# Performance work log

Hardware: AMD Instinct MI355X
Metric: run time of the kernel (lower is better)

## Reference

```python
import jax, jax.numpy as jnp
import numpy as np


def setup_inputs() -> dict:
    key = jax.random.key(0)
    k1, k2 = jax.random.split(key)
    B, C, H, L = 4, 1, 1024, 4096
    x = jax.random.normal(k1, (B, H, L), dtype=jnp.float32)
    k = jax.random.normal(k2, (C, H, L), dtype=jnp.float32)
    return {"x": x, "k": k}


def reference(x, k):
    # x: (B, H, L) input; k: (C, H, l_kernel) SSM convolution kernel.
    # FFT convolution with zero-padding to n = l_kernel + L (linear conv),
    # then truncate to the first L outputs (causal conv output).
    L = x.shape[-1]
    l_kernel = k.shape[-1]
    n = l_kernel + L
    k_f = jnp.fft.rfft(k, n=n)                       # (C, H, n//2+1) complex
    x_f = jnp.fft.rfft(x, n=n)                       # (B, H, n//2+1) complex
    y_f = jnp.einsum('bhl,chl->bchl', x_f, k_f)      # broadcast complex multiply
    y = jnp.fft.irfft(y_f, n=n)[..., :L]             # (B, C, H, L)
    return y
```

## Files before the change

### kernel.cpp

```cpp
#include <hip/hip_runtime.h>

#define THREADS 256
#define B_DIM   4
#define H_DIM   1024
#define L_DIM   4096
#define NFFT    4096
#define PI_F     3.14159265358979323846f
#define TWO_PI_F 6.28318530717958647692f

__device__ __forceinline__ float2 cmulf(float2 a, float2 b) {
    return make_float2(a.x*b.x - a.y*b.y, a.x*b.y + a.y*b.x);
}
__device__ __forceinline__ float2 caddf(float2 a, float2 b){ return make_float2(a.x+b.x, a.y+b.y); }
__device__ __forceinline__ float2 csubf(float2 a, float2 b){ return make_float2(a.x-b.x, a.y-b.y); }

__device__ __forceinline__ int swz(int i) { return i ^ ((i>>4)&15) ^ ((i>>8)&15); }

__device__ __forceinline__ void make_tw(float base, float2 w[16]) {
    float sn, cs; __sincosf(base, &sn, &cs);
    w[1]  = make_float2(cs, sn);
    w[2]  = cmulf(w[1], w[1]);
    w[3]  = cmulf(w[2], w[1]);
    w[4]  = cmulf(w[2], w[2]);
    w[5]  = cmulf(w[4], w[1]);
    w[6]  = cmulf(w[4], w[2]);
    w[7]  = cmulf(w[4], w[3]);
    w[8]  = cmulf(w[4], w[4]);
    w[9]  = cmulf(w[8], w[1]);
    w[10] = cmulf(w[8], w[2]);
    w[11] = cmulf(w[8], w[3]);
    w[12] = cmulf(w[8], w[4]);
    w[13] = cmulf(w[8], w[5]);
    w[14] = cmulf(w[8], w[6]);
    w[15] = cmulf(w[8], w[7]);
}

__device__ __forceinline__ float2 w16c(int q, float s) {
    constexpr float C[8] = {1.f, 0.9238795325f, 0.7071067812f, 0.3826834324f,
                            0.f, -0.3826834324f, -0.7071067812f, -0.9238795325f};
    constexpr float S[8] = {0.f, 0.3826834324f, 0.7071067812f, 0.9238795325f,
                            1.f, 0.9238795325f, 0.7071067812f, 0.3826834324f};
    return make_float2(C[q], s*S[q]);
}

template<int SGN>
__device__ __forceinline__ float2 twq(float2 d, int q) {
    if (q == 0) return d;
    if (q == 4) return make_float2((float)(-SGN)*d.y, (float)SGN*d.x);
    return cmulf(d, w16c(q, (float)SGN));
}

template<int SGN, bool HZ>
__device__ __forceinline__ void dif16(float2 v[16]) {
    if (HZ) {
        #pragma unroll
        for (int i = 0; i < 8; ++i) {
            float2 a = v[i];
            v[i+8] = twq<SGN>(a, i);
        }
    } else {
        #pragma unroll
        for (int i = 0; i < 8; ++i) {
            float2 a = v[i], b = v[i+8];
            v[i]   = caddf(a,b);
            v[i+8] = twq<SGN>(csubf(a,b), i);
        }
    }
    #pragma unroll
    for (int h = 4; h >= 1; h >>= 1) {
        const int step = 8 / h;
        #pragma unroll
        for (int g = 0; g < 16; g += 2*h) {
            #pragma unroll
            for (int i = 0; i < h; ++i) {
                float2 a = v[g+i], b = v[g+i+h];
                v[g+i]   = caddf(a,b);
                v[g+i+h] = twq<SGN>(csubf(a,b), i*step);
            }
        }
    }
}

template<int SGN>
__device__ __forceinline__ void dit16(float2 v[16]) {
    #pragma unroll
    for (int h = 1; h <= 8; h <<= 1) {
        const int step = 8 / h;
        #pragma unroll
        for (int g = 0; g < 16; g += 2*h) {
            #pragma unroll
            for (int i = 0; i < h; ++i) {
                float2 a = v[g+i];
                float2 b = twq<SGN>(v[g+i+h], i*step);
                v[g+i]   = caddf(a,b);
                v[g+i+h] = csubf(a,b);
            }
        }
    }
}

__device__ __constant__ int REV4_C[16] = {0,8,4,12,2,10,6,14,1,9,5,13,3,11,7,15};

__device__ __forceinline__ void fwd_fft_row(const float2* __restrict__ src, float2* Z, int t) {
    constexpr int REV4[16] = {0,8,4,12,2,10,6,14,1,9,5,13,3,11,7,15};
    float2 v[16], w[16];
    #pragma unroll
    for (int r = 0; r < 8; ++r) v[r] = src[256*r + t];
    dif16<-1, true>(v);
    make_tw(-TWO_PI_F * (float)t / (float)NFFT, w);
    #pragma unroll
    for (int kk = 1; kk < 16; ++kk) v[REV4[kk]] = cmulf(v[REV4[kk]], w[kk]);
    #pragma unroll
    for (int kk = 0; kk < 16; ++kk) Z[swz(256*kk + t)] = v[REV4[kk]];
    __syncthreads();

    const int k1 = t >> 4, m = t & 15;
    const int rb = 256*k1 + m;
    #pragma unroll
    for (int r = 0; r < 16; ++r) v[r] = Z[swz(rb + 16*r)];
    dif16<-1,false>(v);
    make_tw(-TWO_PI_F * (float)m / 256.f, w);
    #pragma unroll
    for (int kk = 1; kk < 16; ++kk) v[REV4[kk]] = cmulf(v[REV4[kk]], w[kk]);
    #pragma unroll
    for (int kk = 0; kk < 16; ++kk) Z[swz(rb + 16*kk)] = v[REV4[kk]];
    __syncthreads();

    const int b3 = t << 4;
    #pragma unroll
    for (int r = 0; r < 16; ++r) v[r] = Z[swz(b3 + r)];
    dif16<-1,false>(v);
    #pragma unroll
    for (int kk = 0; kk < 16; ++kk) Z[swz(b3 + kk)] = v[REV4[kk]];
}

__device__ __forceinline__ int binpos(int j) {
    return swz( ((j&15)<<8) | (((j>>4)&15)<<4) | (j>>8) );
}

__global__ __launch_bounds__(THREADS, 4)
void kfft_kernel(const float* __restrict__ k, float2* __restrict__ Kf_all) {
    __shared__ float2 Zk[NFFT];
    const int t  = threadIdx.x;
    const int hh = blockIdx.x;
    const float2* kp = (const float2*)(k + (size_t)hh * L_DIM);

    fwd_fft_row(kp, Zk, t);
    __syncthreads();

    float2* Kf = Kf_all + (size_t)hh * NFFT;
    #pragma unroll
    for (int s = 0; s < 8; ++s) {
        int j = t + 256*s;
        if (j == 0) {
            float2 zk = Zk[0];
            Kf[0] = make_float2(zk.x + zk.y, zk.x - zk.y);
            float2 zk2 = Zk[swz(8)];
            Kf[2048] = make_float2(zk2.x, -zk2.y);
        } else {
            int jm = NFFT - j;
            float2 zkj = Zk[binpos(j)], zkm = Zk[binpos(jm)];
            float sn, cs; __sincosf(-PI_F * (float)j / (float)NFFT, &sn, &cs);
            float2 w = make_float2(cs, sn);
            float2 Ke = make_float2(0.5f*(zkj.x + zkm.x), 0.5f*(zkj.y - zkm.y));
            float2 dk = make_float2(zkj.x - zkm.x, zkj.y + zkm.y);
            float2 Ko = make_float2(0.5f*dk.y, -0.5f*dk.x);
            float2 tk = cmulf(w, Ko);
            Kf[j]  = caddf(Ke, tk);
            Kf[jm] = make_float2(Ke.x - tk.x, -(Ke.y - tk.y));
        }
    }
}

__global__ __launch_bounds__(THREADS, 4)
void conv_main_kernel(const float* __restrict__ x, const float2* __restrict__ Kf_all,
                      float* __restrict__ out) {
    __shared__ float2 Zx[NFFT];
    constexpr int REV4[16] = {0,8,4,12,2,10,6,14,1,9,5,13,3,11,7,15};

    const int t  = threadIdx.x;
    const int wg = blockIdx.x;
    const int hh = wg & (H_DIM - 1);
    const int b  = wg >> 10;

    const float2* xp = (const float2*)(x + ((size_t)(b*H_DIM + hh)) * L_DIM);
    const float2* Kf = Kf_all + (size_t)hh * NFFT;

    fwd_fft_row(xp, Zx, t);

    float2 kfj[8], kfm[8], kf2;
    #pragma unroll
    for (int s = 0; s < 8; ++s) {
        int j = t + 256*s;
        kfj[s] = Kf[j];
        kfm[s] = Kf[(NFFT - j) & (NFFT - 1)];
    }
    kf2 = Kf[2048];
    __syncthreads();

    #pragma unroll
    for (int s = 0; s < 8; ++s) {
        int j = t + 256*s;
        if (j == 0) {
            float2 zx = Zx[0];
            float ax0 = zx.x + zx.y, axM = zx.x - zx.y;
            float y0 = ax0 * kfj[0].x, yM = axM * kfj[0].y;
            Zx[0] = make_float2(0.5f*(y0 + yM), 0.5f*(y0 - yM));
            int p2 = swz(8);
            float2 zx2 = Zx[p2];
            Zx[p2] = cmulf(zx2, make_float2(kf2.x, -kf2.y));
        } else {
            int jm = NFFT - j;
            int pj = binpos(j), pm = binpos(jm);
            float2 zxj = Zx[pj], zxm = Zx[pm];

            float sn, cs; __sincosf(-PI_F * (float)j / (float)NFFT, &sn, &cs);
            float2 w = make_float2(cs, sn);

            float2 Xe = make_float2(0.5f*(zxj.x + zxm.x), 0.5f*(zxj.y - zxm.y));
            float2 dx = make_float2(zxj.x - zxm.x, zxj.y + zxm.y);
            float2 Xo = make_float2(0.5f*dx.y, -0.5f*dx.x);
            float2 tx = cmulf(w, Xo);
            float2 Axj = caddf(Xe, tx);
            float2 Axm = make_float2(Xe.x - tx.x, -(Xe.y - tx.y));

            float2 Yj = cmulf(Axj, kfj[s]);
            float2 Ym = cmulf(Axm, kfm[s]);

            float2 u  = make_float2(0.5f*(Yj.x + Ym.x), 0.5f*(Yj.y - Ym.y));
            float2 dd = make_float2(Yj.x - Ym.x, Yj.y + Ym.y);
            float2 wc = make_float2(w.x, -w.y);
            float2 vv = cmulf(wc, dd);
            vv.x *= 0.5f; vv.y *= 0.5f;
            Zx[pj] = make_float2(u.x - vv.y, u.y + vv.x);
            Zx[pm] = make_float2(u.x + vv.y, -(u.y - vv.x));
        }
    }
    __syncthreads();

    float2 vx[16], w[16];
    const int k1 = t >> 4, m = t & 15;
    const int rb = 256*k1 + m;
    const int b3 = t << 4;

    #pragma unroll
    for (int r = 0; r < 16; ++r) vx[REV4[r]] = Zx[swz(b3 + r)];
    dit16<1>(vx);
    #pragma unroll
    for (int mm = 0; mm < 16; ++mm) Zx[swz(b3 + mm)] = vx[mm];
    __syncthreads();

    make_tw(TWO_PI_F * (float)m / 256.f, w);
    #pragma unroll
    for (int kk = 0; kk < 16; ++kk) {
        float2 val = Zx[swz(rb + 16*kk)];
        if (kk > 0) val = cmulf(val, w[kk]);
        vx[REV4[kk]] = val;
    }
    dit16<1>(vx);
    #pragma unroll
    for (int r = 0; r < 16; ++r) Zx[swz(rb + 16*r)] = vx[r];
    __syncthreads();

    make_tw(TWO_PI_F * (float)t / (float)NFFT, w);
    #pragma unroll
    for (int kk = 0; kk < 16; ++kk) {
        float2 val = Zx[swz(256*kk + t)];
        if (kk > 0) val = cmulf(val, w[kk]);
        vx[REV4[kk]] = val;
    }
    dit16<1>(vx);
    float2* op = (float2*)(out + ((size_t)(b*H_DIM + hh)) * L_DIM);
    const float sc = 1.f / (float)NFFT;
    #pragma unroll
    for (int n1 = 0; n1 < 8; ++n1) {
        float2 z = vx[n1];
        op[256*n1 + t] = make_float2(z.x*sc, z.y*sc);
    }
}

__global__ __launch_bounds__(THREADS, 2)
void fftconv_fallback(const float* __restrict__ x, const float* __restrict__ k,
                      float* __restrict__ out) {
    __shared__ float2 Zx[NFFT];
    __shared__ float2 Zk[NFFT];
    constexpr int REV4[16] = {0,8,4,12,2,10,6,14,1,9,5,13,3,11,7,15};

    const int t  = threadIdx.x;
    const int wg = blockIdx.x;
    const int hh = wg & (H_DIM - 1);
    const int b  = wg >> 10;

    const float2* xp = (const float2*)(x + ((size_t)(b*H_DIM + hh)) * L_DIM);
    const float2* kp = (const float2*)(k + (size_t)hh * L_DIM);

    fwd_fft_row(xp, Zx, t);
    __syncthreads();
    fwd_fft_row(kp, Zk, t);
    __syncthreads();

    #pragma unroll
    for (int s = 0; s < 8; ++s) {
        int j = t + 256*s;
        if (j == 0) {
            float2 zx = Zx[0], zk = Zk[0];
            float ax0 = zx.x + zx.y, axM = zx.x - zx.y;
            float ak0 = zk.x + zk.y, akM = zk.x - zk.y;
            float y0 = ax0*ak0, yM = axM*akM;
            Zx[0] = make_float2(0.5f*(y0+yM), 0.5f*(y0-yM));
            int p2 = swz(8);
            Zx[p2] = cmulf(Zx[p2], Zk[p2]);
        } else {
            int jm = NFFT - j;
            int pj = binpos(j), pm = binpos(jm);
            float2 zxj = Zx[pj], zxm = Zx[pm];
            float2 zkj = Zk[pj], zkm = Zk[pm];
            float sn, cs; __sincosf(-PI_F * (float)j / (float)NFFT, &sn, &cs);
            float2 w = make_float2(cs, sn);
            float2 Xe = make_float2(0.5f*(zxj.x + zxm.x), 0.5f*(zxj.y - zxm.y));
            float2 dx = make_float2(zxj.x - zxm.x, zxj.y + zxm.y);
            float2 Xo = make_float2(0.5f*dx.y, -0.5f*dx.x);
            float2 tx = cmulf(w, Xo);
            float2 Axj = caddf(Xe, tx);
            float2 Axm = make_float2(Xe.x - tx.x, -(Xe.y - tx.y));
            float2 Ke = make_float2(0.5f*(zkj.x + zkm.x), 0.5f*(zkj.y - zkm.y));
            float2 dk = make_float2(zkj.x - zkm.x, zkj.y + zkm.y);
            float2 Ko = make_float2(0.5f*dk.y, -0.5f*dk.x);
            float2 tk = cmulf(w, Ko);
            float2 Akj = caddf(Ke, tk);
            float2 Akm = make_float2(Ke.x - tk.x, -(Ke.y - tk.y));
            float2 Yj = cmulf(Axj, Akj);
            float2 Ym = cmulf(Axm, Akm);
            float2 u  = make_float2(0.5f*(Yj.x + Ym.x), 0.5f*(Yj.y - Ym.y));
            float2 dd = make_float2(Yj.x - Ym.x, Yj.y + Ym.y);
            float2 wc = make_float2(w.x, -w.y);
            float2 vv = cmulf(wc, dd);
            vv.x *= 0.5f; vv.y *= 0.5f;
            Zx[pj] = make_float2(u.x - vv.y, u.y + vv.x);
            Zx[pm] = make_float2(u.x + vv.y, -(u.y - vv.x));
        }
    }
    __syncthreads();

    float2 vx[16], w[16];
    const int k1 = t >> 4, m = t & 15;
    const int rb = 256*k1 + m;
    const int b3 = t << 4;

    #pragma unroll
    for (int r = 0; r < 16; ++r) vx[REV4[r]] = Zx[swz(b3 + r)];
    dit16<1>(vx);
    #pragma unroll
    for (int mm = 0; mm < 16; ++mm) Zx[swz(b3 + mm)] = vx[mm];
    __syncthreads();

    make_tw(TWO_PI_F * (float)m / 256.f, w);
    #pragma unroll
    for (int kk = 0; kk < 16; ++kk) {
        float2 val = Zx[swz(rb + 16*kk)];
        if (kk > 0) val = cmulf(val, w[kk]);
        vx[REV4[kk]] = val;
    }
    dit16<1>(vx);
    #pragma unroll
    for (int r = 0; r < 16; ++r) Zx[swz(rb + 16*r)] = vx[r];
    __syncthreads();

    make_tw(TWO_PI_F * (float)t / (float)NFFT, w);
    #pragma unroll
    for (int kk = 0; kk < 16; ++kk) {
        float2 val = Zx[swz(256*kk + t)];
        if (kk > 0) val = cmulf(val, w[kk]);
        vx[REV4[kk]] = val;
    }
    dit16<1>(vx);
    float2* op = (float2*)(out + ((size_t)(b*H_DIM + hh)) * L_DIM);
    const float sc = 1.f / (float)NFFT;
    #pragma unroll
    for (int n1 = 0; n1 < 8; ++n1) {
        float2 z = vx[n1];
        op[256*n1 + t] = make_float2(z.x*sc, z.y*sc);
    }
}

extern "C" void kernel_launch(void* const* d_in, const int* in_sizes, int n_in,
                              void* d_out, int out_size, void* d_ws, size_t ws_size,
                              hipStream_t stream) {
    const float* x = (const float*)d_in[0];
    const float* k = (const float*)d_in[1];
    float* out = (float*)d_out;
    const size_t need = (size_t)H_DIM * NFFT * sizeof(float2);
    if (ws_size >= need) {
        float2* Kf = (float2*)d_ws;
        kfft_kernel<<<dim3(H_DIM), dim3(THREADS), 0, stream>>>(k, Kf);
        conv_main_kernel<<<dim3(B_DIM * H_DIM), dim3(THREADS), 0, stream>>>(x, Kf, out);
    } else {
        fftconv_fallback<<<dim3(B_DIM * H_DIM), dim3(THREADS), 0, stream>>>(x, k, out);
    }
}
```

Measured before the change: 176.4 us.

## Fuse kernel FFT into conv kernel, looping over batch per head

Replaces the two-kernel scheme (kernel FFT written to workspace, then per-batch conv) with one kernel per head. Each block computes the k spectrum into registers once and reuses it across all four batch rows, which removes the workspace round trip and the second launch. It also replaces the per-bin sincos with a twiddle recurrence and skips the unused upper half of the final inverse butterfly. The cost is that the grid shrinks from 4096 to 1024 blocks with serial batch work per block, which lowers parallelism, and the recurrence may add rounding drift.

```diff
diff --git a/kernel.cpp b/kernel.cpp
--- a/kernel.cpp
+++ b/kernel.cpp
@@ -81,10 +81,10 @@
     }
 }
 
-template<int SGN>
+template<int SGN, bool HALF>
 __device__ __forceinline__ void dit16(float2 v[16]) {
     #pragma unroll
-    for (int h = 1; h <= 8; h <<= 1) {
+    for (int h = 1; h <= 4; h <<= 1) {
         const int step = 8 / h;
         #pragma unroll
         for (int g = 0; g < 16; g += 2*h) {
@@ -97,9 +97,14 @@
             }
         }
     }
-}
-
-__device__ __constant__ int REV4_C[16] = {0,8,4,12,2,10,6,14,1,9,5,13,3,11,7,15};
+    #pragma unroll
+    for (int i = 0; i < 8; ++i) {
+        float2 a = v[i];
+        float2 b = twq<SGN>(v[i+8], i);
+        v[i] = caddf(a,b);
+        if (!HALF) v[i+8] = csubf(a,b);
+    }
+}
 
 __device__ __forceinline__ void fwd_fft_row(const float2* __restrict__ src, float2* Z, int t) {
     constexpr int REV4[16] = {0,8,4,12,2,10,6,14,1,9,5,13,3,11,7,15};
@@ -138,248 +143,138 @@
     return swz( ((j&15)<<8) | (((j>>4)&15)<<4) | (j>>8) );
 }
 
+#define WSTEP_RE 0.980785280403230449f
+#define WSTEP_IM -0.195090322016128268f
+
 __global__ __launch_bounds__(THREADS, 4)
-void kfft_kernel(const float* __restrict__ k, float2* __restrict__ Kf_all) {
-    __shared__ float2 Zk[NFFT];
+void fftconv_fused(const float* __restrict__ x, const float* __restrict__ k,
+                   float* __restrict__ out) {
+    __shared__ float2 Z[NFFT];
+    constexpr int REV4[16] = {0,8,4,12,2,10,6,14,1,9,5,13,3,11,7,15};
+
     const int t  = threadIdx.x;
     const int hh = blockIdx.x;
+
     const float2* kp = (const float2*)(k + (size_t)hh * L_DIM);
-
-    fwd_fft_row(kp, Zk, t);
-    __syncthreads();
-
-    float2* Kf = Kf_all + (size_t)hh * NFFT;
-    #pragma unroll
-    for (int s = 0; s < 8; ++s) {
-        int j = t + 256*s;
-        if (j == 0) {
-            float2 zk = Zk[0];
-            Kf[0] = make_float2(zk.x + zk.y, zk.x - zk.y);
-            float2 zk2 = Zk[swz(8)];
-            Kf[2048] = make_float2(zk2.x, -zk2.y);
-        } else {
-            int jm = NFFT - j;
-            float2 zkj = Zk[binpos(j)], zkm = Zk[binpos(jm)];
-            float sn, cs; __sincosf(-PI_F * (float)j / (float)NFFT, &sn, &cs);
-            float2 w = make_float2(cs, sn);
-            float2 Ke = make_float2(0.5f*(zkj.x + zkm.x), 0.5f*(zkj.y - zkm.y));
-            float2 dk = make_float2(zkj.x - zkm.x, zkj.y + zkm.y);
-            float2 Ko = make_float2(0.5f*dk.y, -0.5f*dk.x);
-            float2 tk = cmulf(w, Ko);
-            Kf[j]  = caddf(Ke, tk);
-            Kf[jm] = make_float2(Ke.x - tk.x, -(Ke.y - tk.y));
-        }
-    }
-}
-
-__global__ __launch_bounds__(THREADS, 4)
-void conv_main_kernel(const float* __restrict__ x, const float2* __restrict__ Kf_all,
-                      float* __restrict__ out) {
-    __shared__ float2 Zx[NFFT];
-    constexpr int REV4[16] = {0,8,4,12,2,10,6,14,1,9,5,13,3,11,7,15};
-
-    const int t  = threadIdx.x;
-    const int wg = blockIdx.x;
-    const int hh = wg & (H_DIM - 1);
-    const int b  = wg >> 10;
-
-    const float2* xp = (const float2*)(x + ((size_t)(b*H_DIM + hh)) * L_DIM);
-    const float2* Kf = Kf_all + (size_t)hh * NFFT;
-
-    fwd_fft_row(xp, Zx, t);
+    fwd_fft_row(kp, Z, t);
+    __syncthreads();
 
     float2 kfj[8], kfm[8], kf2;
-    #pragma unroll
-    for (int s = 0; s < 8; ++s) {
-        int j = t + 256*s;
-        kfj[s] = Kf[j];
-        kfm[s] = Kf[(NFFT - j) & (NFFT - 1)];
-    }
-    kf2 = Kf[2048];
-    __syncthreads();
-
-    #pragma unroll
-    for (int s = 0; s < 8; ++s) {
-        int j = t + 256*s;
-        if (j == 0) {
-            float2 zx = Zx[0];
-            float ax0 = zx.x + zx.y, axM = zx.x - zx.y;
-            float y0 = ax0 * kfj[0].x, yM = axM * kfj[0].y;
-            Zx[0] = make_float2(0.5f*(y0 + yM), 0.5f*(y0 - yM));
-            int p2 = swz(8);
-            float2 zx2 = Zx[p2];
-            Zx[p2] = cmulf(zx2, make_float2(kf2.x, -kf2.y));
-        } else {
-            int jm = NFFT - j;
-            int pj = binpos(j), pm = binpos(jm);
-            float2 zxj = Zx[pj], zxm = Zx[pm];
-
-            float sn, cs; __sincosf(-PI_F * (float)j / (float)NFFT, &sn, &cs);
-            float2 w = make_float2(cs, sn);
-
-            float2 Xe = make_float2(0.5f*(zxj.x + zxm.x), 0.5f*(zxj.y - zxm.y));
-            float2 dx = make_float2(zxj.x - zxm.x, zxj.y + zxm.y);
-            float2 Xo = make_float2(0.5f*dx.y, -0.5f*dx.x);
-            float2 tx = cmulf(w, Xo);
-            float2 Axj = caddf(Xe, tx);
-            float2 Axm = make_float2(Xe.x - tx.x, -(Xe.y - tx.y));
-
-            float2 Yj = cmulf(Axj, kfj[s]);
-            float2 Ym = cmulf(Axm, kfm[s]);
-
-            float2 u  = make_float2(0.5f*(Yj.x + Ym.x), 0.5f*(Yj.y - Ym.y));
-            float2 dd = make_float2(Yj.x - Ym.x, Yj.y + Ym.y);
-            float2 wc = make_float2(w.x, -w.y);
-            float2 vv = cmulf(wc, dd);
-            vv.x *= 0.5f; vv.y *= 0.5f;
-            Zx[pj] = make_float2(u.x - vv.y, u.y + vv.x);
-            Zx[pm] = make_float2(u.x + vv.y, -(u.y - vv.x));
-        }
-    }
-    __syncthreads();
-
-    float2 vx[16], w[16];
+    {
+        float sn, cs; __sincosf(-PI_F * (float)t / (float)NFFT, &sn, &cs);
+        float2 wj = make_float2(cs, sn);
+        const float2 WS = make_float2(WSTEP_RE, WSTEP_IM);
+        kf2 = Z[swz(8)];
+        #pragma unroll
+        for (int s = 0; s < 8; ++s) {
+            int j = t + 256*s;
+            if (j == 0) {
+                float2 zk = Z[0];
+                kfj[0] = make_float2(zk.x + zk.y, zk.x - zk.y);
+                kfm[0] = make_float2(0.f, 0.f);
+            } else {
+                int jm = NFFT - j;
+                float2 zkj = Z[binpos(j)], zkm = Z[binpos(jm)];
+                float2 Ke = make_float2(0.5f*(zkj.x + zkm.x), 0.5f*(zkj.y - zkm.y));
+                float2 dk = make_float2(zkj.x - zkm.x, zkj.y + zkm.y);
+                float2 Ko = make_float2(0.5f*dk.y, -0.5f*dk.x);
+                float2 tk = cmulf(wj, Ko);
+                kfj[s] = caddf(Ke, tk);
+                kfm[s] = make_float2(Ke.x - tk.x, -(Ke.y - tk.y));
+            }
+            wj = cmulf(wj, WS);
+        }
+    }
+    __syncthreads();
+
     const int k1 = t >> 4, m = t & 15;
     const int rb = 256*k1 + m;
     const int b3 = t << 4;
 
-    #pragma unroll
-    for (int r = 0; r < 16; ++r) vx[REV4[r]] = Zx[swz(b3 + r)];
-    dit16<1>(vx);
-    #pragma unroll
-    for (int mm = 0; mm < 16; ++mm) Zx[swz(b3 + mm)] = vx[mm];
-    __syncthreads();
-
-    make_tw(TWO_PI_F * (float)m / 256.f, w);
-    #pragma unroll
-    for (int kk = 0; kk < 16; ++kk) {
-        float2 val = Zx[swz(rb + 16*kk)];
-        if (kk > 0) val = cmulf(val, w[kk]);
-        vx[REV4[kk]] = val;
-    }
-    dit16<1>(vx);
-    #pragma unroll
-    for (int r = 0; r < 16; ++r) Zx[swz(rb + 16*r)] = vx[r];
-    __syncthreads();
-
-    make_tw(TWO_PI_F * (float)t / (float)NFFT, w);
-    #pragma unroll
-    for (int kk = 0; kk < 16; ++kk) {
-        float2 val = Zx[swz(256*kk + t)];
-        if (kk > 0) val = cmulf(val, w[kk]);
-        vx[REV4[kk]] = val;
-    }
-    dit16<1>(vx);
-    float2* op = (float2*)(out + ((size_t)(b*H_DIM + hh)) * L_DIM);
-    const float sc = 1.f / (float)NFFT;
-    #pragma unroll
-    for (int n1 = 0; n1 < 8; ++n1) {
-        float2 z = vx[n1];
-        op[256*n1 + t] = make_float2(z.x*sc, z.y*sc);
-    }
-}
-
-__global__ __launch_bounds__(THREADS, 2)
-void fftconv_fallback(const float* __restrict__ x, const float* __restrict__ k,
-                      float* __restrict__ out) {
-    __shared__ float2 Zx[NFFT];
-    __shared__ float2 Zk[NFFT];
-    constexpr int REV4[16] = {0,8,4,12,2,10,6,14,1,9,5,13,3,11,7,15};
-
-    const int t  = threadIdx.x;
-    const int wg = blockIdx.x;
-    const int hh = wg & (H_DIM - 1);
-    const int b  = wg >> 10;
-
-    const float2* xp = (const float2*)(x + ((size_t)(b*H_DIM + hh)) * L_DIM);
-    const float2* kp = (const float2*)(k + (size_t)hh * L_DIM);
-
-    fwd_fft_row(xp, Zx, t);
-    __syncthreads();
-    fwd_fft_row(kp, Zk, t);
-    __syncthreads();
-
-    #pragma unroll
-    for (int s = 0; s < 8; ++s) {
-        int j = t + 256*s;
-        if (j == 0) {
-            float2 zx = Zx[0], zk = Zk[0];
-            float ax0 = zx.x + zx.y, axM = zx.x - zx.y;
-            float ak0 = zk.x + zk.y, akM = zk.x - zk.y;
-            float y0 = ax0*ak0, yM = axM*akM;
-            Zx[0] = make_float2(0.5f*(y0+yM), 0.5f*(y0-yM));
-            int p2 = swz(8);
-            Zx[p2] = cmulf(Zx[p2], Zk[p2]);
-        } else {
-            int jm = NFFT - j;
-            int pj = binpos(j), pm = binpos(jm);
-            float2 zxj = Zx[pj], zxm = Zx[pm];
-            float2 zkj = Zk[pj], zkm = Zk[pm];
-            float sn, cs; __sincosf(-PI_F * (float)j / (float)NFFT, &sn, &cs);
-            float2 w = make_float2(cs, sn);
-            float2 Xe = make_float2(0.5f*(zxj.x + zxm.x), 0.5f*(zxj.y - zxm.y));
-            float2 dx = make_float2(zxj.x - zxm.x, zxj.y + zxm.y);
-            float2 Xo = make_float2(0.5f*dx.y, -0.5f*dx.x);
-            float2 tx = cmulf(w, Xo);
-            float2 Axj = caddf(Xe, tx);
-            float2 Axm = make_float2(Xe.x - tx.x, -(Xe.y - tx.y));
-            float2 Ke = make_float2(0.5f*(zkj.x + zkm.x), 0.5f*(zkj.y - zkm.y));
-            float2 dk = make_float2(zkj.x - zkm.x, zkj.y + zkm.y);
-            float2 Ko = make_float2(0.5f*dk.y, -0.5f*dk.x);
-            float2 tk = cmulf(w, Ko);
-            float2 Akj = caddf(Ke, tk);
-            float2 Akm = make_float2(Ke.x - tk.x, -(Ke.y - tk.y));
-            float2 Yj = cmulf(Axj, Akj);
-            float2 Ym = cmulf(Axm, Akm);
-            float2 u  = make_float2(0.5f*(Yj.x + Ym.x), 0.5f*(Yj.y - Ym.y));
-            float2 dd = make_float2(Yj.x - Ym.x, Yj.y + Ym.y);
-            float2 wc = make_float2(w.x, -w.y);
-            float2 vv = cmulf(wc, dd);
-            vv.x *= 0.5f; vv.y *= 0.5f;
-            Zx[pj] = make_float2(u.x - vv.y, u.y + vv.x);
-            Zx[pm] = make_float2(u.x + vv.y, -(u.y - vv.x));
-        }
-    }
-    __syncthreads();
-
-    float2 vx[16], w[16];
-    const int k1 = t >> 4, m = t & 15;
-    const int rb = 256*k1 + m;
-    const int b3 = t << 4;
-
-    #pragma unroll
-    for (int r = 0; r < 16; ++r) vx[REV4[r]] = Zx[swz(b3 + r)];
-    dit16<1>(vx);
-    #pragma unroll
-    for (int mm = 0; mm < 16; ++mm) Zx[swz(b3 + mm)] = vx[mm];
-    __syncthreads();
-
-    make_tw(TWO_PI_F * (float)m / 256.f, w);
-    #pragma unroll
-    for (int kk = 0; kk < 16; ++kk) {
-        float2 val = Zx[swz(rb + 16*kk)];
-        if (kk > 0) val = cmulf(val, w[kk]);
-        vx[REV4[kk]] = val;
-    }
-    dit16<1>(vx);
-    #pragma unroll
-    for (int r = 0; r < 16; ++r) Zx[swz(rb + 16*r)] = vx[r];
-    __syncthreads();
-
-    make_tw(TWO_PI_F * (float)t / (float)NFFT, w);
-    #pragma unroll
-    for (int kk = 0; kk < 16; ++kk) {
-        float2 val = Zx[swz(256*kk + t)];
-        if (kk > 0) val = cmulf(val, w[kk]);
-        vx[REV4[kk]] = val;
-    }
-    dit16<1>(vx);
-    float2* op = (float2*)(out + ((size_t)(b*H_DIM + hh)) * L_DIM);
-    const float sc = 1.f / (float)NFFT;
-    #pragma unroll
-    for (int n1 = 0; n1 < 8; ++n1) {
-        float2 z = vx[n1];
-        op[256*n1 + t] = make_float2(z.x*sc, z.y*sc);
+    for (int b = 0; b < B_DIM; ++b) {
+        const float2* xp = (const float2*)(x + ((size_t)(b*H_DIM + hh)) * L_DIM);
+        fwd_fft_row(xp, Z, t);
+        __syncthreads();
+
+        {
+            float sn, cs; __sincosf(-PI_F * (float)t / (float)NFFT, &sn, &cs);
+            float2 wj = make_float2(cs, sn);
+            const float2 WS = make_float2(WSTEP_RE, WSTEP_IM);
+            #pragma unroll
+            for (int s = 0; s < 8; ++s) {
+                int j = t + 256*s;
+                if (j == 0) {
+                    float2 zx = Z[0];
+                    float ax0 = zx.x + zx.y, axM = zx.x - zx.y;
+                    float y0 = ax0 * kfj[0].x, yM = axM * kfj[0].y;
+                    Z[0] = make_float2(0.5f*(y0 + yM), 0.5f*(y0 - yM));
+                    int p2 = swz(8);
+                    Z[p2] = cmulf(Z[p2], kf2);
+                } else {
+                    int jm = NFFT - j;
+                    int pj = binpos(j), pm = binpos(jm);
+                    float2 zxj = Z[pj], zxm = Z[pm];
+
+                    float2 Xe = make_float2(0.5f*(zxj.x + zxm.x), 0.5f*(zxj.y - zxm.y));
+                    float2 dx = make_float2(zxj.x - zxm.x, zxj.y + zxm.y);
+                    float2 Xo = make_float2(0.5f*dx.y, -0.5f*dx.x);
+                    float2 tx = cmulf(wj, Xo);
+                    float2 Axj = caddf(Xe, tx);
+                    float2 Axm = make_float2(Xe.x - tx.x, -(Xe.y - tx.y));
+
+                    float2 Yj = cmulf(Axj, kfj[s]);
+                    float2 Ym = cmulf(Axm, kfm[s]);
+
+                    float2 u  = make_float2(0.5f*(Yj.x + Ym.x), 0.5f*(Yj.y - Ym.y));
+                    float2 dd = make_float2(Yj.x - Ym.x, Yj.y + Ym.y);
+                    float2 wc = make_float2(wj.x, -wj.y);
+                    float2 vv = cmulf(wc, dd);
+                    vv.x *= 0.5f; vv.y *= 0.5f;
+                    Z[pj] = make_float2(u.x - vv.y, u.y + vv.x);
+                    Z[pm] = make_float2(u.x + vv.y, -(u.y - vv.x));
+                }
+                wj = cmulf(wj, WS);
+            }
+        }
+        __syncthreads();
+
+        float2 vx[16], w[16];
+
+        #pragma unroll
+        for (int r = 0; r < 16; ++r) vx[REV4[r]] = Z[swz(b3 + r)];
+        dit16<1,false>(vx);
+        #pragma unroll
+        for (int mm = 0; mm < 16; ++mm) Z[swz(b3 + mm)] = vx[mm];
+        __syncthreads();
+
+        make_tw(TWO_PI_F * (float)m / 256.f, w);
+        #pragma unroll
+        for (int kk = 0; kk < 16; ++kk) {
+            float2 val = Z[swz(rb + 16*kk)];
+            if (kk > 0) val = cmulf(val, w[kk]);
+            vx[REV4[kk]] = val;
+        }
+        dit16<1,false>(vx);
+        #pragma unroll
+        for (int r = 0; r < 16; ++r) Z[swz(rb + 16*r)] = vx[r];
+        __syncthreads();
+
+        make_tw(TWO_PI_F * (float)t / (float)NFFT, w);
+        #pragma unroll
+        for (int kk = 0; kk < 16; ++kk) {
+            float2 val = Z[swz(256*kk + t)];
+            if (kk > 0) val = cmulf(val, w[kk]);
+            vx[REV4[kk]] = val;
+        }
+        dit16<1,true>(vx);
+        float2* op = (float2*)(out + ((size_t)(b*H_DIM + hh)) * L_DIM);
+        const float sc = 1.f / (float)NFFT;
+        #pragma unroll
+        for (int n1 = 0; n1 < 8; ++n1) {
+            float2 z = vx[n1];
+            op[256*n1 + t] = make_float2(z.x*sc, z.y*sc);
+        }
+        __syncthreads();
     }
 }
 
@@ -389,12 +284,5 @@
     const float* x = (const float*)d_in[0];
     const float* k = (const float*)d_in[1];
     float* out = (float*)d_out;
-    const size_t need = (size_t)H_DIM * NFFT * sizeof(float2);
-    if (ws_size >= need) {
-        float2* Kf = (float2*)d_ws;
-        kfft_kernel<<<dim3(H_DIM), dim3(THREADS), 0, stream>>>(k, Kf);
-        conv_main_kernel<<<dim3(B_DIM * H_DIM), dim3(THREADS), 0, stream>>>(x, Kf, out);
-    } else {
-        fftconv_fallback<<<dim3(B_DIM * H_DIM), dim3(THREADS), 0, stream>>>(x, k, out);
-    }
-}
+    fftconv_fused<<<dim3(H_DIM), dim3(THREADS), 0, stream>>>(x, k, out);
+}
```

Result: slower. 652.5 us (+269.9%).
